# Optimization experiments

Hardware: AMD Instinct MI355X
Metric: run time of the kernel (lower is better)

## Reference

```python
import jax, jax.numpy as jnp
import numpy as np
from jax import lax

NX, NW, NY, NLAYER = 128, 64, 32, 2
NWUP, NBATCH, NHRZN = 256, 1024, 256


def setup_inputs() -> dict:
    key = jax.random.key(0)
    ks = jax.random.split(key, 18)
    s = 0.05
    n = lambda k, shp: jax.random.normal(k, shp, jnp.float32) * s
    return {
        "_Y0": jax.random.normal(ks[0], (NWUP + 1, NBATCH, NY), jnp.float32),
        # q_x_y: Linear(Ny, Nx*Nlayer) + Tanh
        "Wq": n(ks[1], (NX * NLAYER, NY)), "bq": n(ks[2], (NX * NLAYER,)),
        # p_y_x: Linear(Nx,Nx)+Tanh+Linear(Nx,Ny)
        "Wp1": n(ks[3], (NX, NX)), "bp1": n(ks[4], (NX,)),
        "Wp2": n(ks[5], (NY, NX)), "bp2": n(ks[6], (NY,)),
        # q_w_xy: Linear(Nx+Ny, Nw)+Tanh
        "Ww": n(ks[7], (NW, NX + NY)), "bw": n(ks[8], (NW,)),
        # GRU layer 0 (input Nw) and layer 1 (input Nx), PyTorch gate order r,z,n
        "Wih0": n(ks[9], (3 * NX, NW)), "Whh0": n(ks[10], (3 * NX, NX)),
        "bih0": n(ks[11], (3 * NX,)), "bhh0": n(ks[12], (3 * NX,)),
        "Wih1": n(ks[13], (3 * NX, NX)), "Whh1": n(ks[14], (3 * NX, NX)),
        "bih1": n(ks[15], (3 * NX,)), "bhh1": n(ks[16], (3 * NX,)),
        "Nhrzn": NHRZN,
    }


def _gru_cell(x, h, Wih, Whh, bih, bhh):
    # PyTorch GRUCell math, gate order (r, z, n)
    gi = x @ Wih.T + bih
    gh = h @ Whh.T + bhh
    ir, iz, inn = jnp.split(gi, 3, axis=-1)
    hr, hz, hn = jnp.split(gh, 3, axis=-1)
    r = jax.nn.sigmoid(ir + hr)
    z = jax.nn.sigmoid(iz + hz)
    ng = jnp.tanh(inn + r * hn)
    return (1.0 - z) * ng + z * h


def reference(_Y0, Wq, bq, Wp1, bp1, Wp2, bp2, Ww, bw,
              Wih0, Whh0, bih0, bhh0, Wih1, Whh1, bih1, bhh1, Nhrzn):
    Nwup = _Y0.shape[0] - 1
    B, Ny = _Y0.shape[1], _Y0.shape[2]
    Nlayer = Wq.shape[0] // Wp1.shape[0]
    Nx = Wp1.shape[0]

    p_y_x = lambda h: jnp.tanh(h @ Wp1.T + bp1) @ Wp2.T + bp2

    # initial multi-layer hidden state (Nlayer, B, Nx)
    x0 = jnp.tanh(_Y0[0] @ Wq.T + bq).reshape(B, Nlayer, Nx).transpose(1, 0, 2)
    yhat0 = p_y_x(x0[-1])

    T = Nwup + Nhrzn
    y_seq = jnp.concatenate(
        [_Y0[1:], jnp.zeros((Nhrzn, B, Ny), _Y0.dtype)], axis=0)  # (T, B, Ny)
    wup_mask = (jnp.arange(T) < Nwup).astype(_Y0.dtype)  # training branch: w=0 in horizon

    def step(carry, inp):
        x, yhat = carry  # x: (Nlayer, B, Nx)
        y_t, m = inp
        e = y_t - yhat
        w = jnp.tanh(jnp.concatenate([x[0], e], axis=-1) @ Ww.T + bw) * m
        h0 = _gru_cell(w, x[0], Wih0, Whh0, bih0, bhh0)
        h1 = _gru_cell(h0, x[1], Wih1, Whh1, bih1, bhh1)
        x_new = jnp.stack([h0, h1], axis=0)
        yhat_new = p_y_x(h1)
        return (x_new, yhat_new), (h1, w, yhat_new)

    _, (Xs, Ws, Ys) = lax.scan(step, (x0, yhat0), (y_seq, wup_mask))

    X = jnp.concatenate([x0[-1][None], Xs], axis=0)      # (T+1, B, Nx)
    Yhat = jnp.concatenate([yhat0[None], Ys], axis=0)    # (T+1, B, Ny)
    W = Ws[:Nwup]                                        # (Nwup, B, Nw)
    return X, W, Yhat
```

## Files before the change

kernel.cpp:

```cpp
#include <hip/hip_runtime.h>

#define NBATCH 1024
#define TSTEPS 512
#define NWUPC  256

#define XLEN 67239936ULL
#define WLEN 16777216ULL

typedef __attribute__((ext_vector_type(8))) short bf16x8;
typedef __attribute__((ext_vector_type(4))) float f32x4;

__device__ __forceinline__ unsigned short to_bf16u(float f) {
  union { float f; unsigned u; } v; v.f = f;
  unsigned r = (v.u + 0x7FFFu + ((v.u >> 16) & 1u)) >> 16;
  return (unsigned short)r;
}
__device__ __forceinline__ float bf16_to_f(short h) {
  union { unsigned u; float f; } v;
  v.u = ((unsigned)(unsigned short)h) << 16;
  return v.f;
}
__device__ __forceinline__ float sigm(float x) {
  x = fminf(fmaxf(x, -30.f), 30.f);
  return __builtin_amdgcn_rcpf(1.f + __expf(-x));
}
__device__ __forceinline__ float ftanh(float x) {
  x = fminf(fmaxf(x, -15.f), 15.f);
  float e = __expf(2.f * x);
  return (e - 1.f) * __builtin_amdgcn_rcpf(e + 1.f);
}

__device__ __forceinline__ void fast_barrier() {
  __builtin_amdgcn_sched_barrier(0);
  asm volatile("s_waitcnt lgkmcnt(0)" ::: "memory");
  __builtin_amdgcn_s_barrier();
  __builtin_amdgcn_sched_barrier(0);
}

#define MFMA16(a, b, c) __builtin_amdgcn_mfma_f32_16x16x32_bf16((a), (b), (c), 0, 0, 0)

__device__ __forceinline__ bf16x8 load_wfrag(const float* __restrict__ W, int ldk,
                                             int rowbase, int kbase, int cl, int rg) {
  const float* p = W + (size_t)(rowbase + cl) * (size_t)ldk + (size_t)(kbase + rg * 8);
  float4 a = *reinterpret_cast<const float4*>(p);
  float4 b = *reinterpret_cast<const float4*>(p + 4);
  bf16x8 r;
  r[0] = (short)to_bf16u(a.x); r[1] = (short)to_bf16u(a.y);
  r[2] = (short)to_bf16u(a.z); r[3] = (short)to_bf16u(a.w);
  r[4] = (short)to_bf16u(b.x); r[5] = (short)to_bf16u(b.y);
  r[6] = (short)to_bf16u(b.z); r[7] = (short)to_bf16u(b.w);
  return r;
}

template <int ROWB, int SLOTS>
__device__ __forceinline__ bf16x8 lds_afrag(const unsigned short* buf, int kt, int cl, int rg) {
  int chunk = (kt * 4 + rg) ^ (cl & (SLOTS - 1));
  return *reinterpret_cast<const bf16x8*>(
      reinterpret_cast<const char*>(buf) + cl * ROWB + chunk * 16);
}

template <int ROWB, int SLOTS>
__device__ __forceinline__ void store_c_lds(unsigned short* buf, int colbase, f32x4 v,
                                            int cl, int rg) {
#pragma unroll
  for (int r = 0; r < 4; ++r) {
    int row = rg * 4 + r;
    int col = colbase + cl;
    int chunk = (col >> 3) ^ (row & (SLOTS - 1));
    *reinterpret_cast<unsigned short*>(
        reinterpret_cast<char*>(buf) + row * ROWB + chunk * 16 + (col & 7) * 2) =
        to_bf16u(v[r]);
  }
}

__device__ __forceinline__ void store_c_glb(float* __restrict__ base, int ld, int colbase,
                                            f32x4 v, int cl, int rg) {
#pragma unroll
  for (int r = 0; r < 4; ++r) base[(rg * 4 + r) * ld + colbase + cl] = v[r];
}

__device__ __forceinline__ bf16x8 read_pfrag(const unsigned short* buf, int f, int lane) {
  return *reinterpret_cast<const bf16x8*>(buf + f * 512 + lane * 8);
}

__global__ __launch_bounds__(512, 2) void sinkbf_kernel(
    const float* __restrict__ Y0, const float* __restrict__ Wq, const float* __restrict__ bq,
    const float* __restrict__ Wp1, const float* __restrict__ bp1,
    const float* __restrict__ Wp2, const float* __restrict__ bp2,
    const float* __restrict__ Ww, const float* __restrict__ bw,
    const float* __restrict__ Wih0, const float* __restrict__ Whh0,
    const float* __restrict__ bih0, const float* __restrict__ bhh0,
    const float* __restrict__ Wih1, const float* __restrict__ Whh1,
    const float* __restrict__ bih1, const float* __restrict__ bhh1,
    float* __restrict__ outX, float* __restrict__ outW, float* __restrict__ outY) {
  const int tid = threadIdx.x;
  const int wid = tid >> 6;
  const int lane = tid & 63;
  const int cl = lane & 15;
  const int rg = lane >> 4;
  const int row0 = blockIdx.x * 16;
  const int c0 = wid * 16;

  __shared__ __align__(16) unsigned short sH0[2][16 * 128];
  __shared__ __align__(16) unsigned short sH1[2][16 * 128];
  __shared__ __align__(16) unsigned short sWb[16 * 64];
  __shared__ __align__(16) unsigned short sT[16 * 128];
  __shared__ __align__(16) unsigned short sYh[16 * 32];
  __shared__ __align__(16) unsigned short sWwP[20 * 512];
  __shared__ __align__(16) unsigned short sWp1P[32 * 512];
  __shared__ __align__(16) unsigned short sWp2P[8 * 512];

  const f32x4 vzero = {0.f, 0.f, 0.f, 0.f};

  bf16x8 wI0[3][2];
  bf16x8 wH0[3][4];
  bf16x8 wI1[3][4];
  bf16x8 wH1[3][4];
#pragma unroll
  for (int g = 0; g < 3; ++g) {
    int rb = g * 128 + c0;
#pragma unroll
    for (int kt = 0; kt < 2; ++kt) wI0[g][kt] = load_wfrag(Wih0, 64, rb, kt * 32, cl, rg);
#pragma unroll
    for (int kt = 0; kt < 4; ++kt) wH0[g][kt] = load_wfrag(Whh0, 128, rb, kt * 32, cl, rg);
#pragma unroll
    for (int kt = 0; kt < 4; ++kt) wI1[g][kt] = load_wfrag(Wih1, 128, rb, kt * 32, cl, rg);
#pragma unroll
    for (int kt = 0; kt < 4; ++kt) wH1[g][kt] = load_wfrag(Whh1, 128, rb, kt * 32, cl, rg);
  }

  if (wid < 4) {
#pragma unroll
    for (int kt = 0; kt < 5; ++kt) {
      bf16x8 f = load_wfrag(Ww, 160, wid * 16, kt * 32, cl, rg);
      *reinterpret_cast<bf16x8*>(&sWwP[(wid * 5 + kt) * 512 + lane * 8]) = f;
    }
  }
#pragma unroll
  for (int kt = 0; kt < 4; ++kt) {
    bf16x8 f = load_wfrag(Wp1, 128, c0, kt * 32, cl, rg);
    *reinterpret_cast<bf16x8*>(&sWp1P[(wid * 4 + kt) * 512 + lane * 8]) = f;
  }
  if (wid < 2) {
#pragma unroll
    for (int kt = 0; kt < 4; ++kt) {
      bf16x8 f = load_wfrag(Wp2, 128, wid * 16, kt * 32, cl, rg);
      *reinterpret_cast<bf16x8*>(&sWp2P[(wid * 4 + kt) * 512 + lane * 8]) = f;
    }
  }

  const int c = c0 + cl;
  const float b0r = bih0[c] + bhh0[c];
  const float b0z = bih0[128 + c] + bhh0[128 + c];
  const float b0in = bih0[256 + c];
  const float b0hn = bhh0[256 + c];
  const float b1r = bih1[c] + bhh1[c];
  const float b1z = bih1[128 + c] + bhh1[128 + c];
  const float b1in = bih1[256 + c];
  const float b1hn = bhh1[256 + c];
  const float bp1l = bp1[c];
  const float bwl = bw[(wid & 3) * 16 + cl];
  const float bp2l = (wid < 2) ? bp2[wid * 16 + cl] : 0.f;

  f32x4 hp0, hp1;

  {
    bf16x8 aY = load_wfrag(Y0, 32, row0, 0, cl, rg);
    bf16x8 q0 = load_wfrag(Wq, 32, c0, 0, cl, rg);
    bf16x8 q1 = load_wfrag(Wq, 32, 128 + c0, 0, cl, rg);
    float bq0v = bq[c];
    float bq1v = bq[128 + c];
    f32x4 acc = MFMA16(aY, q0, vzero);
#pragma unroll
    for (int r = 0; r < 4; ++r) hp0[r] = ftanh(acc[r] + bq0v);
    store_c_lds<256, 8>(sH0[0], c0, hp0, cl, rg);
    acc = MFMA16(aY, q1, vzero);
#pragma unroll
    for (int r = 0; r < 4; ++r) hp1[r] = ftanh(acc[r] + bq1v);
    store_c_lds<256, 8>(sH1[0], c0, hp1, cl, rg);
    store_c_glb(outX + (size_t)row0 * 128, 128, c0, hp1, cl, rg);
  }
  __syncthreads();

  float4 yA, yB;
  if (wid < 4) {
    const float* py = Y0 + (size_t)1 * (NBATCH * 32) + (size_t)(row0 + cl) * 32 + rg * 8;
    yA = *reinterpret_cast<const float4*>(py);
    yB = *reinterpret_cast<const float4*>(py + 4);
  }

  auto p_phase = [&](int tout, const unsigned short* h1buf) {
    bf16x8 a1[4];
#pragma unroll
    for (int kt = 0; kt < 4; ++kt) a1[kt] = lds_afrag<256, 8>(h1buf, kt, cl, rg);
    f32x4 acc = vzero;
#pragma unroll
    for (int kt = 0; kt < 4; ++kt)
      acc = MFMA16(a1[kt], read_pfrag(sWp1P, wid * 4 + kt, lane), acc);
    f32x4 tv;
#pragma unroll
    for (int r = 0; r < 4; ++r) tv[r] = ftanh(acc[r] + bp1l);
    store_c_lds<256, 8>(sT, c0, tv, cl, rg);
    fast_barrier();
    if (wid < 2) {
      bf16x8 at[4];
#pragma unroll
      for (int kt = 0; kt < 4; ++kt) at[kt] = lds_afrag<256, 8>(sT, kt, cl, rg);
      f32x4 acc2 = vzero;
#pragma unroll
      for (int kt = 0; kt < 4; ++kt) acc2 = MFMA16(at[kt], read_pfrag(sWp2P, wid * 4 + kt, lane), acc2);
      f32x4 y;
#pragma unroll
      for (int r = 0; r < 4; ++r) y[r] = acc2[r] + bp2l;
      store_c_glb(outY + (size_t)tout * (NBATCH * 32) + (size_t)row0 * 32, 32, wid * 16, y, cl, rg);
      store_c_lds<64, 4>(sYh, wid * 16, y, cl, rg);
    }
    fast_barrier();
  };

  p_phase(0, sH1[0]);

#pragma unroll 1
  for (int t = 0; t < TSTEPS; ++t) {
    const int cur = t & 1, nxt = cur ^ 1;
    const unsigned short* h0c = sH0[cur];
    unsigned short* h0w = sH0[nxt];
    const unsigned short* h1c = sH1[cur];
    unsigned short* h1w = sH1[nxt];
    const bool warm = (t < NWUPC);

    bf16x8 aH0[4];
#pragma unroll
    for (int kt = 0; kt < 4; ++kt) aH0[kt] = lds_afrag<256, 8>(h0c, kt, cl, rg);

    if (warm) {
      if (wid < 4) {
        bf16x8 ae;
        {
          int chunk = rg ^ (cl & 3);
          bf16x8 yh = *reinterpret_cast<const bf16x8*>(
              reinterpret_cast<const char*>(sYh) + cl * 64 + chunk * 16);
          ae[0] = (short)to_bf16u(yA.x - bf16_to_f(yh[0]));
          ae[1] = (short)to_bf16u(yA.y - bf16_to_f(yh[1]));
          ae[2] = (short)to_bf16u(yA.z - bf16_to_f(yh[2]));
          ae[3] = (short)to_bf16u(yA.w - bf16_to_f(yh[3]));
          ae[4] = (short)to_bf16u(yB.x - bf16_to_f(yh[4]));
          ae[5] = (short)to_bf16u(yB.y - bf16_to_f(yh[5]));
          ae[6] = (short)to_bf16u(yB.z - bf16_to_f(yh[6]));
          ae[7] = (short)to_bf16u(yB.w - bf16_to_f(yh[7]));
        }
        if (t + 1 < NWUPC) {
          const float* py = Y0 + (size_t)(2 + t) * (NBATCH * 32) + (size_t)(row0 + cl) * 32 + rg * 8;
          yA = *reinterpret_cast<const float4*>(py);
          yB = *reinterpret_cast<const float4*>(py + 4);
        }
        f32x4 acc = vzero;
#pragma unroll
        for (int kt = 0; kt < 4; ++kt)
          acc = MFMA16(aH0[kt], read_pfrag(sWwP, wid * 5 + kt, lane), acc);
        acc = MFMA16(ae, read_pfrag(sWwP, wid * 5 + 4, lane), acc);
        f32x4 wv;
#pragma unroll
        for (int r = 0; r < 4; ++r) wv[r] = ftanh(acc[r] + bwl);
        store_c_lds<128, 8>(sWb, wid * 16, wv, cl, rg);
        store_c_glb(outW + (size_t)t * (NBATCH * 64) + (size_t)row0 * 64, 64, wid * 16, wv, cl, rg);
      }
      fast_barrier();
    }

    f32x4 ar0 = vzero, az0 = vzero, ain0 = vzero, ahn0 = vzero;
    if (warm) {
      bf16x8 aw0 = lds_afrag<128, 8>(sWb, 0, cl, rg);
      bf16x8 aw1 = lds_afrag<128, 8>(sWb, 1, cl, rg);
      ar0 = MFMA16(aw0, wI0[0][0], ar0);  ar0 = MFMA16(aw1, wI0[0][1], ar0);
      az0 = MFMA16(aw0, wI0[1][0], az0);  az0 = MFMA16(aw1, wI0[1][1], az0);
      ain0 = MFMA16(aw0, wI0[2][0], ain0); ain0 = MFMA16(aw1, wI0[2][1], ain0);
    }
#pragma unroll
    for (int kt = 0; kt < 4; ++kt) {
      ar0 = MFMA16(aH0[kt], wH0[0][kt], ar0);
      az0 = MFMA16(aH0[kt], wH0[1][kt], az0);
      ahn0 = MFMA16(aH0[kt], wH0[2][kt], ahn0);
    }
    f32x4 h0new;
#pragma unroll
    for (int r = 0; r < 4; ++r) {
      float rr = sigm(ar0[r] + b0r);
      float zz = sigm(az0[r] + b0z);
      float ng = ftanh(ain0[r] + b0in + rr * (ahn0[r] + b0hn));
      h0new[r] = (1.f - zz) * ng + zz * hp0[r];
    }
    store_c_lds<256, 8>(h0w, c0, h0new, cl, rg);
    hp0 = h0new;
    fast_barrier();

    bf16x8 aH0n[4], aH1[4];
#pragma unroll
    for (int kt = 0; kt < 4; ++kt) aH0n[kt] = lds_afrag<256, 8>(h0w, kt, cl, rg);
#pragma unroll
    for (int kt = 0; kt < 4; ++kt) aH1[kt] = lds_afrag<256, 8>(h1c, kt, cl, rg);
    f32x4 ar1 = vzero, az1 = vzero, ain1 = vzero, ahn1 = vzero;
#pragma unroll
    for (int kt = 0; kt < 4; ++kt) {
      ar1 = MFMA16(aH0n[kt], wI1[0][kt], ar1);
      az1 = MFMA16(aH0n[kt], wI1[1][kt], az1);
      ain1 = MFMA16(aH0n[kt], wI1[2][kt], ain1);
      ar1 = MFMA16(aH1[kt], wH1[0][kt], ar1);
      az1 = MFMA16(aH1[kt], wH1[1][kt], az1);
      ahn1 = MFMA16(aH1[kt], wH1[2][kt], ahn1);
    }
    f32x4 h1new;
#pragma unroll
    for (int r = 0; r < 4; ++r) {
      float rr = sigm(ar1[r] + b1r);
      float zz = sigm(az1[r] + b1z);
      float ng = ftanh(ain1[r] + b1in + rr * (ahn1[r] + b1hn));
      h1new[r] = (1.f - zz) * ng + zz * hp1[r];
    }
    store_c_lds<256, 8>(h1w, c0, h1new, cl, rg);
    store_c_glb(outX + (size_t)(1 + t) * (NBATCH * 128) + (size_t)row0 * 128, 128,
                c0, h1new, cl, rg);
    hp1 = h1new;
    fast_barrier();

    if (warm) p_phase(1 + t, h1w);
  }
}

__global__ __launch_bounds__(256, 1) void yhat_hrzn_kernel(
    const float* __restrict__ X, const float* __restrict__ Wp1, const float* __restrict__ bp1,
    const float* __restrict__ Wp2, const float* __restrict__ bp2, float* __restrict__ outY) {
  const int tid = threadIdx.x;
  const int wid = tid >> 6;
  const int lane = tid & 63;
  const int cl = lane & 15;
  const int rg = lane >> 4;
  const int tile = blockIdx.x & 63;
  const int tg = blockIdx.x >> 6;
  const int row0 = tile * 16;
  const int c0 = wid * 32;

  __shared__ __align__(16) unsigned short sT2[2][16 * 128];
  const f32x4 vzero = {0.f, 0.f, 0.f, 0.f};

  bf16x8 wp1f[2][4];
#pragma unroll
  for (int tl = 0; tl < 2; ++tl)
#pragma unroll
    for (int kt = 0; kt < 4; ++kt) wp1f[tl][kt] = load_wfrag(Wp1, 128, c0 + tl * 16, kt * 32, cl, rg);
  bf16x8 wp2f[4];
  if (wid < 2) {
#pragma unroll
    for (int kt = 0; kt < 4; ++kt) wp2f[kt] = load_wfrag(Wp2, 128, wid * 16, kt * 32, cl, rg);
  } else {
#pragma unroll
    for (int kt = 0; kt < 4; ++kt) wp2f[kt] = bf16x8{0, 0, 0, 0, 0, 0, 0, 0};
  }
  float bp1l[2] = {bp1[c0 + cl], bp1[c0 + 16 + cl]};
  const float bp2l = (wid < 2) ? bp2[wid * 16 + cl] : 0.f;

#pragma unroll 1
  for (int i = 0; i < 4; ++i) {
    const int tt = 257 + tg * 4 + i;
    const float* xb = X + (size_t)tt * (NBATCH * 128);
    bf16x8 aX[4];
#pragma unroll
    for (int kt = 0; kt < 4; ++kt) aX[kt] = load_wfrag(xb, 128, row0, kt * 32, cl, rg);
#pragma unroll
    for (int tl = 0; tl < 2; ++tl) {
      f32x4 acc = vzero;
#pragma unroll
      for (int kt = 0; kt < 4; ++kt) acc = MFMA16(aX[kt], wp1f[tl][kt], acc);
      f32x4 tv;
#pragma unroll
      for (int r = 0; r < 4; ++r) tv[r] = ftanh(acc[r] + bp1l[tl]);
      store_c_lds<256, 8>(sT2[i & 1], c0 + tl * 16, tv, cl, rg);
    }
    __syncthreads();
    if (wid < 2) {
      bf16x8 at[4];
#pragma unroll
      for (int kt = 0; kt < 4; ++kt) at[kt] = lds_afrag<256, 8>(sT2[i & 1], kt, cl, rg);
      f32x4 acc = vzero;
#pragma unroll
      for (int kt = 0; kt < 4; ++kt) acc = MFMA16(at[kt], wp2f[kt], acc);
      f32x4 y;
#pragma unroll
      for (int r = 0; r < 4; ++r) y[r] = acc[r] + bp2l;
      store_c_glb(outY + (size_t)tt * (NBATCH * 32) + (size_t)row0 * 32, 32, wid * 16, y, cl, rg);
    }
  }
}

extern "C" void kernel_launch(void* const* d_in, const int* in_sizes, int n_in,
                              void* d_out, int out_size, void* d_ws, size_t ws_size,
                              hipStream_t stream) {
  (void)in_sizes; (void)n_in; (void)out_size; (void)d_ws; (void)ws_size;
  const float* Y0   = (const float*)d_in[0];
  const float* Wq   = (const float*)d_in[1];
  const float* bq   = (const float*)d_in[2];
  const float* Wp1  = (const float*)d_in[3];
  const float* bp1  = (const float*)d_in[4];
  const float* Wp2  = (const float*)d_in[5];
  const float* bp2  = (const float*)d_in[6];
  const float* Ww   = (const float*)d_in[7];
  const float* bw   = (const float*)d_in[8];
  const float* Wih0 = (const float*)d_in[9];
  const float* Whh0 = (const float*)d_in[10];
  const float* bih0 = (const float*)d_in[11];
  const float* bhh0 = (const float*)d_in[12];
  const float* Wih1 = (const float*)d_in[13];
  const float* Whh1 = (const float*)d_in[14];
  const float* bih1 = (const float*)d_in[15];
  const float* bhh1 = (const float*)d_in[16];

  float* outX = (float*)d_out;
  float* outW = outX + XLEN;
  float* outY = outW + WLEN;

  sinkbf_kernel<<<dim3(NBATCH / 16), dim3(512), 0, stream>>>(
      Y0, Wq, bq, Wp1, bp1, Wp2, bp2, Ww, bw,
      Wih0, Whh0, bih0, bhh0, Wih1, Whh1, bih1, bhh1,
      outX, outW, outY);

  yhat_hrzn_kernel<<<dim3(64 * 64), dim3(256), 0, stream>>>(
      outX, Wp1, bp1, Wp2, bp2, outY);
}
```

Before: 1.933 ms.

## Fold Wp2 into the innovation weight to cut yhat from the recurrent critical path

Because yhat is linear in the tanh hidden activation T, the error term e = y - yhat is rewritten algebraically. The Ww error block is premultiplied by -Wp2 and the bias is adjusted, so w is computed directly from y and T without first computing yhat. This removes the second Wp2 MFMA stage and one barrier from each recurrent step. The yhat output is now computed by spare waves 4-5 in parallel, and the horizon kernel picks up one extra timestep (with an extra block group and a bounds check). The trade-offs are a small change in bf16 rounding, a precompute of the folded weights at kernel start, and larger LDS use.

```diff
diff --git a/kernel.cpp b/kernel.cpp
--- a/kernel.cpp
+++ b/kernel.cpp
@@ -105,10 +105,8 @@
   __shared__ __align__(16) unsigned short sH1[2][16 * 128];
   __shared__ __align__(16) unsigned short sWb[16 * 64];
   __shared__ __align__(16) unsigned short sT[16 * 128];
-  __shared__ __align__(16) unsigned short sYh[16 * 32];
-  __shared__ __align__(16) unsigned short sWwP[20 * 512];
+  __shared__ __align__(16) unsigned short sWwP[36 * 512];
   __shared__ __align__(16) unsigned short sWp1P[32 * 512];
-  __shared__ __align__(16) unsigned short sWp2P[8 * 512];
 
   const f32x4 vzero = {0.f, 0.f, 0.f, 0.f};
 
@@ -131,9 +129,31 @@
 
   if (wid < 4) {
 #pragma unroll
-    for (int kt = 0; kt < 5; ++kt) {
+    for (int kt = 0; kt < 4; ++kt) {
       bf16x8 f = load_wfrag(Ww, 160, wid * 16, kt * 32, cl, rg);
-      *reinterpret_cast<bf16x8*>(&sWwP[(wid * 5 + kt) * 512 + lane * 8]) = f;
+      *reinterpret_cast<bf16x8*>(&sWwP[(wid * 9 + kt) * 512 + lane * 8]) = f;
+    }
+    {
+      bf16x8 f = load_wfrag(Ww, 160, wid * 16, 128, cl, rg);
+      *reinterpret_cast<bf16x8*>(&sWwP[(wid * 9 + 4) * 512 + lane * 8]) = f;
+    }
+    {
+      float wwc[32];
+#pragma unroll 8
+      for (int c = 0; c < 32; ++c) wwc[c] = Ww[(wid * 16 + cl) * 160 + 128 + c];
+#pragma unroll
+      for (int kt = 0; kt < 4; ++kt) {
+        bf16x8 f;
+#pragma unroll
+        for (int v = 0; v < 8; ++v) {
+          int k = kt * 32 + rg * 8 + v;
+          float s = 0.f;
+#pragma unroll 8
+          for (int c = 0; c < 32; ++c) s += Wp2[c * 128 + k] * wwc[c];
+          f[v] = (short)to_bf16u(-s);
+        }
+        *reinterpret_cast<bf16x8*>(&sWwP[(wid * 9 + 5 + kt) * 512 + lane * 8]) = f;
+      }
     }
   }
 #pragma unroll
@@ -141,12 +161,13 @@
     bf16x8 f = load_wfrag(Wp1, 128, c0, kt * 32, cl, rg);
     *reinterpret_cast<bf16x8*>(&sWp1P[(wid * 4 + kt) * 512 + lane * 8]) = f;
   }
-  if (wid < 2) {
-#pragma unroll
-    for (int kt = 0; kt < 4; ++kt) {
-      bf16x8 f = load_wfrag(Wp2, 128, wid * 16, kt * 32, cl, rg);
-      *reinterpret_cast<bf16x8*>(&sWp2P[(wid * 4 + kt) * 512 + lane * 8]) = f;
-    }
+  bf16x8 wp2f[4];
+  if (wid == 4 || wid == 5) {
+#pragma unroll
+    for (int kt = 0; kt < 4; ++kt) wp2f[kt] = load_wfrag(Wp2, 128, (wid - 4) * 16, kt * 32, cl, rg);
+  } else {
+#pragma unroll
+    for (int kt = 0; kt < 4; ++kt) wp2f[kt] = bf16x8{0, 0, 0, 0, 0, 0, 0, 0};
   }
 
   const int c = c0 + cl;
@@ -159,8 +180,14 @@
   const float b1in = bih1[256 + c];
   const float b1hn = bhh1[256 + c];
   const float bp1l = bp1[c];
-  const float bwl = bw[(wid & 3) * 16 + cl];
-  const float bp2l = (wid < 2) ? bp2[wid * 16 + cl] : 0.f;
+  float bwl = 0.f;
+  if (wid < 4) {
+    float s = bw[wid * 16 + cl];
+#pragma unroll 8
+    for (int cc = 0; cc < 32; ++cc) s -= bp2[cc] * Ww[(wid * 16 + cl) * 160 + 128 + cc];
+    bwl = s;
+  }
+  const float bp2l = (wid == 4 || wid == 5) ? bp2[(wid - 4) * 16 + cl] : 0.f;
 
   f32x4 hp0, hp1;
 
@@ -182,6 +209,20 @@
   }
   __syncthreads();
 
+  {
+    bf16x8 a1[4];
+#pragma unroll
+    for (int kt = 0; kt < 4; ++kt) a1[kt] = lds_afrag<256, 8>(sH1[0], kt, cl, rg);
+    f32x4 acc = vzero;
+#pragma unroll
+    for (int kt = 0; kt < 4; ++kt) acc = MFMA16(a1[kt], read_pfrag(sWp1P, wid * 4 + kt, lane), acc);
+    f32x4 tv;
+#pragma unroll
+    for (int r = 0; r < 4; ++r) tv[r] = ftanh(acc[r] + bp1l);
+    store_c_lds<256, 8>(sT, c0, tv, cl, rg);
+  }
+  fast_barrier();
+
   float4 yA, yB;
   if (wid < 4) {
     const float* py = Y0 + (size_t)1 * (NBATCH * 32) + (size_t)(row0 + cl) * 32 + rg * 8;
@@ -189,36 +230,9 @@
     yB = *reinterpret_cast<const float4*>(py + 4);
   }
 
-  auto p_phase = [&](int tout, const unsigned short* h1buf) {
-    bf16x8 a1[4];
-#pragma unroll
-    for (int kt = 0; kt < 4; ++kt) a1[kt] = lds_afrag<256, 8>(h1buf, kt, cl, rg);
-    f32x4 acc = vzero;
-#pragma unroll
-    for (int kt = 0; kt < 4; ++kt)
-      acc = MFMA16(a1[kt], read_pfrag(sWp1P, wid * 4 + kt, lane), acc);
-    f32x4 tv;
-#pragma unroll
-    for (int r = 0; r < 4; ++r) tv[r] = ftanh(acc[r] + bp1l);
-    store_c_lds<256, 8>(sT, c0, tv, cl, rg);
-    fast_barrier();
-    if (wid < 2) {
-      bf16x8 at[4];
-#pragma unroll
-      for (int kt = 0; kt < 4; ++kt) at[kt] = lds_afrag<256, 8>(sT, kt, cl, rg);
-      f32x4 acc2 = vzero;
-#pragma unroll
-      for (int kt = 0; kt < 4; ++kt) acc2 = MFMA16(at[kt], read_pfrag(sWp2P, wid * 4 + kt, lane), acc2);
-      f32x4 y;
-#pragma unroll
-      for (int r = 0; r < 4; ++r) y[r] = acc2[r] + bp2l;
-      store_c_glb(outY + (size_t)tout * (NBATCH * 32) + (size_t)row0 * 32, 32, wid * 16, y, cl, rg);
-      store_c_lds<64, 4>(sYh, wid * 16, y, cl, rg);
-    }
-    fast_barrier();
-  };
-
-  p_phase(0, sH1[0]);
+  float* pX = outX + (size_t)(NBATCH * 128) + (size_t)row0 * 128;
+  float* pW = outW + (size_t)row0 * 64;
+  float* pY = outY + (size_t)row0 * 32;
 
 #pragma unroll 1
   for (int t = 0; t < TSTEPS; ++t) {
@@ -235,58 +249,67 @@
 
     if (warm) {
       if (wid < 4) {
-        bf16x8 ae;
-        {
-          int chunk = rg ^ (cl & 3);
-          bf16x8 yh = *reinterpret_cast<const bf16x8*>(
-              reinterpret_cast<const char*>(sYh) + cl * 64 + chunk * 16);
-          ae[0] = (short)to_bf16u(yA.x - bf16_to_f(yh[0]));
-          ae[1] = (short)to_bf16u(yA.y - bf16_to_f(yh[1]));
-          ae[2] = (short)to_bf16u(yA.z - bf16_to_f(yh[2]));
-          ae[3] = (short)to_bf16u(yA.w - bf16_to_f(yh[3]));
-          ae[4] = (short)to_bf16u(yB.x - bf16_to_f(yh[4]));
-          ae[5] = (short)to_bf16u(yB.y - bf16_to_f(yh[5]));
-          ae[6] = (short)to_bf16u(yB.z - bf16_to_f(yh[6]));
-          ae[7] = (short)to_bf16u(yB.w - bf16_to_f(yh[7]));
-        }
+        bf16x8 tf[4];
+#pragma unroll
+        for (int kt = 0; kt < 4; ++kt) tf[kt] = lds_afrag<256, 8>(sT, kt, cl, rg);
+        bf16x8 ay;
+        ay[0] = (short)to_bf16u(yA.x); ay[1] = (short)to_bf16u(yA.y);
+        ay[2] = (short)to_bf16u(yA.z); ay[3] = (short)to_bf16u(yA.w);
+        ay[4] = (short)to_bf16u(yB.x); ay[5] = (short)to_bf16u(yB.y);
+        ay[6] = (short)to_bf16u(yB.z); ay[7] = (short)to_bf16u(yB.w);
         if (t + 1 < NWUPC) {
           const float* py = Y0 + (size_t)(2 + t) * (NBATCH * 32) + (size_t)(row0 + cl) * 32 + rg * 8;
           yA = *reinterpret_cast<const float4*>(py);
           yB = *reinterpret_cast<const float4*>(py + 4);
         }
+        f32x4 accA = MFMA16(ay, read_pfrag(sWwP, wid * 9 + 4, lane), vzero);
+#pragma unroll
+        for (int kt = 0; kt < 4; ++kt)
+          accA = MFMA16(aH0[kt], read_pfrag(sWwP, wid * 9 + kt, lane), accA);
+        f32x4 accB = vzero;
+#pragma unroll
+        for (int kt = 0; kt < 4; ++kt)
+          accB = MFMA16(tf[kt], read_pfrag(sWwP, wid * 9 + 5 + kt, lane), accB);
+        f32x4 wv;
+#pragma unroll
+        for (int r = 0; r < 4; ++r) wv[r] = ftanh(accA[r] + accB[r] + bwl);
+        store_c_lds<128, 8>(sWb, wid * 16, wv, cl, rg);
+        store_c_glb(pW, 64, wid * 16, wv, cl, rg);
+      } else if (wid < 6) {
+        bf16x8 tf[4];
+#pragma unroll
+        for (int kt = 0; kt < 4; ++kt) tf[kt] = lds_afrag<256, 8>(sT, kt, cl, rg);
         f32x4 acc = vzero;
 #pragma unroll
-        for (int kt = 0; kt < 4; ++kt)
-          acc = MFMA16(aH0[kt], read_pfrag(sWwP, wid * 5 + kt, lane), acc);
-        acc = MFMA16(ae, read_pfrag(sWwP, wid * 5 + 4, lane), acc);
-        f32x4 wv;
-#pragma unroll
-        for (int r = 0; r < 4; ++r) wv[r] = ftanh(acc[r] + bwl);
-        store_c_lds<128, 8>(sWb, wid * 16, wv, cl, rg);
-        store_c_glb(outW + (size_t)t * (NBATCH * 64) + (size_t)row0 * 64, 64, wid * 16, wv, cl, rg);
+        for (int kt = 0; kt < 4; ++kt) acc = MFMA16(tf[kt], wp2f[kt], acc);
+        f32x4 y;
+#pragma unroll
+        for (int r = 0; r < 4; ++r) y[r] = acc[r] + bp2l;
+        store_c_glb(pY, 32, (wid - 4) * 16, y, cl, rg);
       }
       fast_barrier();
     }
 
-    f32x4 ar0 = vzero, az0 = vzero, ain0 = vzero, ahn0 = vzero;
+    f32x4 ar0i = vzero, az0i = vzero, ain0 = vzero;
     if (warm) {
       bf16x8 aw0 = lds_afrag<128, 8>(sWb, 0, cl, rg);
       bf16x8 aw1 = lds_afrag<128, 8>(sWb, 1, cl, rg);
-      ar0 = MFMA16(aw0, wI0[0][0], ar0);  ar0 = MFMA16(aw1, wI0[0][1], ar0);
-      az0 = MFMA16(aw0, wI0[1][0], az0);  az0 = MFMA16(aw1, wI0[1][1], az0);
-      ain0 = MFMA16(aw0, wI0[2][0], ain0); ain0 = MFMA16(aw1, wI0[2][1], ain0);
-    }
+      ar0i = MFMA16(aw0, wI0[0][0], ar0i);  ar0i = MFMA16(aw1, wI0[0][1], ar0i);
+      az0i = MFMA16(aw0, wI0[1][0], az0i);  az0i = MFMA16(aw1, wI0[1][1], az0i);
+      ain0 = MFMA16(aw0, wI0[2][0], ain0);  ain0 = MFMA16(aw1, wI0[2][1], ain0);
+    }
+    f32x4 ar0h = vzero, az0h = vzero, ahn0 = vzero;
 #pragma unroll
     for (int kt = 0; kt < 4; ++kt) {
-      ar0 = MFMA16(aH0[kt], wH0[0][kt], ar0);
-      az0 = MFMA16(aH0[kt], wH0[1][kt], az0);
+      ar0h = MFMA16(aH0[kt], wH0[0][kt], ar0h);
+      az0h = MFMA16(aH0[kt], wH0[1][kt], az0h);
       ahn0 = MFMA16(aH0[kt], wH0[2][kt], ahn0);
     }
     f32x4 h0new;
 #pragma unroll
     for (int r = 0; r < 4; ++r) {
-      float rr = sigm(ar0[r] + b0r);
-      float zz = sigm(az0[r] + b0z);
+      float rr = sigm(ar0i[r] + ar0h[r] + b0r);
+      float zz = sigm(az0i[r] + az0h[r] + b0z);
       float ng = ftanh(ain0[r] + b0in + rr * (ahn0[r] + b0hn));
       h0new[r] = (1.f - zz) * ng + zz * hp0[r];
     }
@@ -299,31 +322,47 @@
     for (int kt = 0; kt < 4; ++kt) aH0n[kt] = lds_afrag<256, 8>(h0w, kt, cl, rg);
 #pragma unroll
     for (int kt = 0; kt < 4; ++kt) aH1[kt] = lds_afrag<256, 8>(h1c, kt, cl, rg);
-    f32x4 ar1 = vzero, az1 = vzero, ain1 = vzero, ahn1 = vzero;
+    f32x4 ar1i = vzero, az1i = vzero, ain1 = vzero;
+    f32x4 ar1h = vzero, az1h = vzero, ahn1 = vzero;
 #pragma unroll
     for (int kt = 0; kt < 4; ++kt) {
-      ar1 = MFMA16(aH0n[kt], wI1[0][kt], ar1);
-      az1 = MFMA16(aH0n[kt], wI1[1][kt], az1);
+      ar1i = MFMA16(aH0n[kt], wI1[0][kt], ar1i);
+      az1i = MFMA16(aH0n[kt], wI1[1][kt], az1i);
       ain1 = MFMA16(aH0n[kt], wI1[2][kt], ain1);
-      ar1 = MFMA16(aH1[kt], wH1[0][kt], ar1);
-      az1 = MFMA16(aH1[kt], wH1[1][kt], az1);
+      ar1h = MFMA16(aH1[kt], wH1[0][kt], ar1h);
+      az1h = MFMA16(aH1[kt], wH1[1][kt], az1h);
       ahn1 = MFMA16(aH1[kt], wH1[2][kt], ahn1);
     }
     f32x4 h1new;
 #pragma unroll
     for (int r = 0; r < 4; ++r) {
-      float rr = sigm(ar1[r] + b1r);
-      float zz = sigm(az1[r] + b1z);
+      float rr = sigm(ar1i[r] + ar1h[r] + b1r);
+      float zz = sigm(az1i[r] + az1h[r] + b1z);
       float ng = ftanh(ain1[r] + b1in + rr * (ahn1[r] + b1hn));
       h1new[r] = (1.f - zz) * ng + zz * hp1[r];
     }
     store_c_lds<256, 8>(h1w, c0, h1new, cl, rg);
-    store_c_glb(outX + (size_t)(1 + t) * (NBATCH * 128) + (size_t)row0 * 128, 128,
-                c0, h1new, cl, rg);
+    store_c_glb(pX, 128, c0, h1new, cl, rg);
     hp1 = h1new;
     fast_barrier();
 
-    if (warm) p_phase(1 + t, h1w);
+    if (t + 1 < NWUPC) {
+      bf16x8 a1[4];
+#pragma unroll
+      for (int kt = 0; kt < 4; ++kt) a1[kt] = lds_afrag<256, 8>(h1w, kt, cl, rg);
+      f32x4 acc = vzero;
+#pragma unroll
+      for (int kt = 0; kt < 4; ++kt) acc = MFMA16(a1[kt], read_pfrag(sWp1P, wid * 4 + kt, lane), acc);
+      f32x4 tv;
+#pragma unroll
+      for (int r = 0; r < 4; ++r) tv[r] = ftanh(acc[r] + bp1l);
+      store_c_lds<256, 8>(sT, c0, tv, cl, rg);
+      fast_barrier();
+    }
+
+    pX += NBATCH * 128;
+    pW += NBATCH * 64;
+    pY += NBATCH * 32;
   }
 }
 
@@ -361,7 +400,8 @@
 
 #pragma unroll 1
   for (int i = 0; i < 4; ++i) {
-    const int tt = 257 + tg * 4 + i;
+    const int tt = 256 + tg * 4 + i;
+    if (tt > 512) break;
     const float* xb = X + (size_t)tt * (NBATCH * 128);
     bf16x8 aX[4];
 #pragma unroll
@@ -389,6 +429,7 @@
       for (int r = 0; r < 4; ++r) y[r] = acc[r] + bp2l;
       store_c_glb(outY + (size_t)tt * (NBATCH * 32) + (size_t)row0 * 32, 32, wid * 16, y, cl, rg);
     }
+    __syncthreads();
   }
 }
 
@@ -423,6 +464,6 @@
       Wih0, Whh0, bih0, bhh0, Wih1, Whh1, bih1, bhh1,
       outX, outW, outY);
 
-  yhat_hrzn_kernel<<<dim3(64 * 64), dim3(256), 0, stream>>>(
+  yhat_hrzn_kernel<<<dim3(64 * 65), dim3(256), 0, stream>>>(
       outX, Wp1, bp1, Wp2, bp2, outY);
 }
```

Measured after the change: 2.031 ms. 5.1% more time.

## Split GRU gate accumulators and hoist h1 fragment loads off the critical path

Applied to the files above, without the earlier changes.

Moves the layer-1 hidden-state LDS fragment loads to the start of the step and splits the input and hidden gate accumulators into separate MFMA chains. This lets the h-dependent MFMAs issue before the barrier-gated input contributions are ready, shortening the serial dependency per step. It also drops the clamps in sigmoid/tanh, relaxes the sched_barrier masks around the block barrier, and replaces per-step output address arithmetic with incremented pointers. Removing the clamps risks inf/NaN handling edge cases, and the extra live fragment registers raise register pressure.

```diff
diff --git a/kernel.cpp b/kernel.cpp
--- a/kernel.cpp
+++ b/kernel.cpp
@@ -21,20 +21,17 @@
   return v.f;
 }
 __device__ __forceinline__ float sigm(float x) {
-  x = fminf(fmaxf(x, -30.f), 30.f);
   return __builtin_amdgcn_rcpf(1.f + __expf(-x));
 }
 __device__ __forceinline__ float ftanh(float x) {
-  x = fminf(fmaxf(x, -15.f), 15.f);
   float e = __expf(2.f * x);
   return (e - 1.f) * __builtin_amdgcn_rcpf(e + 1.f);
 }
 
 __device__ __forceinline__ void fast_barrier() {
-  __builtin_amdgcn_sched_barrier(0);
   asm volatile("s_waitcnt lgkmcnt(0)" ::: "memory");
   __builtin_amdgcn_s_barrier();
-  __builtin_amdgcn_sched_barrier(0);
+  __builtin_amdgcn_sched_barrier(0xF);
 }
 
 #define MFMA16(a, b, c) __builtin_amdgcn_mfma_f32_16x16x32_bf16((a), (b), (c), 0, 0, 0)
@@ -189,7 +186,11 @@
     yB = *reinterpret_cast<const float4*>(py + 4);
   }
 
-  auto p_phase = [&](int tout, const unsigned short* h1buf) {
+  float* pX = outX + (size_t)(NBATCH * 128) + (size_t)row0 * 128;
+  float* pW = outW + (size_t)row0 * 64;
+  float* pY = outY + (size_t)row0 * 32;
+
+  auto p_phase = [&](float* yout, const unsigned short* h1buf) {
     bf16x8 a1[4];
 #pragma unroll
     for (int kt = 0; kt < 4; ++kt) a1[kt] = lds_afrag<256, 8>(h1buf, kt, cl, rg);
@@ -212,13 +213,14 @@
       f32x4 y;
 #pragma unroll
       for (int r = 0; r < 4; ++r) y[r] = acc2[r] + bp2l;
-      store_c_glb(outY + (size_t)tout * (NBATCH * 32) + (size_t)row0 * 32, 32, wid * 16, y, cl, rg);
+      store_c_glb(yout, 32, wid * 16, y, cl, rg);
       store_c_lds<64, 4>(sYh, wid * 16, y, cl, rg);
     }
     fast_barrier();
   };
 
-  p_phase(0, sH1[0]);
+  p_phase(pY, sH1[0]);
+  pY += NBATCH * 32;
 
 #pragma unroll 1
   for (int t = 0; t < TSTEPS; ++t) {
@@ -229,9 +231,11 @@
     unsigned short* h1w = sH1[nxt];
     const bool warm = (t < NWUPC);
 
-    bf16x8 aH0[4];
+    bf16x8 aH0[4], aH1[4];
 #pragma unroll
     for (int kt = 0; kt < 4; ++kt) aH0[kt] = lds_afrag<256, 8>(h0c, kt, cl, rg);
+#pragma unroll
+    for (int kt = 0; kt < 4; ++kt) aH1[kt] = lds_afrag<256, 8>(h1c, kt, cl, rg);
 
     if (warm) {
       if (wid < 4) {
@@ -263,30 +267,31 @@
 #pragma unroll
         for (int r = 0; r < 4; ++r) wv[r] = ftanh(acc[r] + bwl);
         store_c_lds<128, 8>(sWb, wid * 16, wv, cl, rg);
-        store_c_glb(outW + (size_t)t * (NBATCH * 64) + (size_t)row0 * 64, 64, wid * 16, wv, cl, rg);
+        store_c_glb(pW, 64, wid * 16, wv, cl, rg);
       }
       fast_barrier();
     }
 
-    f32x4 ar0 = vzero, az0 = vzero, ain0 = vzero, ahn0 = vzero;
+    f32x4 ar0i = vzero, az0i = vzero, ain0 = vzero;
     if (warm) {
       bf16x8 aw0 = lds_afrag<128, 8>(sWb, 0, cl, rg);
       bf16x8 aw1 = lds_afrag<128, 8>(sWb, 1, cl, rg);
-      ar0 = MFMA16(aw0, wI0[0][0], ar0);  ar0 = MFMA16(aw1, wI0[0][1], ar0);
-      az0 = MFMA16(aw0, wI0[1][0], az0);  az0 = MFMA16(aw1, wI0[1][1], az0);
-      ain0 = MFMA16(aw0, wI0[2][0], ain0); ain0 = MFMA16(aw1, wI0[2][1], ain0);
-    }
+      ar0i = MFMA16(aw0, wI0[0][0], ar0i);  ar0i = MFMA16(aw1, wI0[0][1], ar0i);
+      az0i = MFMA16(aw0, wI0[1][0], az0i);  az0i = MFMA16(aw1, wI0[1][1], az0i);
+      ain0 = MFMA16(aw0, wI0[2][0], ain0);  ain0 = MFMA16(aw1, wI0[2][1], ain0);
+    }
+    f32x4 ar0h = vzero, az0h = vzero, ahn0 = vzero;
 #pragma unroll
     for (int kt = 0; kt < 4; ++kt) {
-      ar0 = MFMA16(aH0[kt], wH0[0][kt], ar0);
-      az0 = MFMA16(aH0[kt], wH0[1][kt], az0);
+      ar0h = MFMA16(aH0[kt], wH0[0][kt], ar0h);
+      az0h = MFMA16(aH0[kt], wH0[1][kt], az0h);
       ahn0 = MFMA16(aH0[kt], wH0[2][kt], ahn0);
     }
     f32x4 h0new;
 #pragma unroll
     for (int r = 0; r < 4; ++r) {
-      float rr = sigm(ar0[r] + b0r);
-      float zz = sigm(az0[r] + b0z);
+      float rr = sigm(ar0i[r] + ar0h[r] + b0r);
+      float zz = sigm(az0i[r] + az0h[r] + b0z);
       float ng = ftanh(ain0[r] + b0in + rr * (ahn0[r] + b0hn));
       h0new[r] = (1.f - zz) * ng + zz * hp0[r];
     }
@@ -294,36 +299,40 @@
     hp0 = h0new;
     fast_barrier();
 
-    bf16x8 aH0n[4], aH1[4];
+    bf16x8 aH0n[4];
 #pragma unroll
     for (int kt = 0; kt < 4; ++kt) aH0n[kt] = lds_afrag<256, 8>(h0w, kt, cl, rg);
-#pragma unroll
-    for (int kt = 0; kt < 4; ++kt) aH1[kt] = lds_afrag<256, 8>(h1c, kt, cl, rg);
-    f32x4 ar1 = vzero, az1 = vzero, ain1 = vzero, ahn1 = vzero;
+    f32x4 ar1i = vzero, az1i = vzero, ain1 = vzero;
+    f32x4 ar1h = vzero, az1h = vzero, ahn1 = vzero;
 #pragma unroll
     for (int kt = 0; kt < 4; ++kt) {
-      ar1 = MFMA16(aH0n[kt], wI1[0][kt], ar1);
-      az1 = MFMA16(aH0n[kt], wI1[1][kt], az1);
+      ar1h = MFMA16(aH1[kt], wH1[0][kt], ar1h);
+      az1h = MFMA16(aH1[kt], wH1[1][kt], az1h);
+      ahn1 = MFMA16(aH1[kt], wH1[2][kt], ahn1);
+      ar1i = MFMA16(aH0n[kt], wI1[0][kt], ar1i);
+      az1i = MFMA16(aH0n[kt], wI1[1][kt], az1i);
       ain1 = MFMA16(aH0n[kt], wI1[2][kt], ain1);
-      ar1 = MFMA16(aH1[kt], wH1[0][kt], ar1);
-      az1 = MFMA16(aH1[kt], wH1[1][kt], az1);
-      ahn1 = MFMA16(aH1[kt], wH1[2][kt], ahn1);
     }
     f32x4 h1new;
 #pragma unroll
     for (int r = 0; r < 4; ++r) {
-      float rr = sigm(ar1[r] + b1r);
-      float zz = sigm(az1[r] + b1z);
+      float rr = sigm(ar1i[r] + ar1h[r] + b1r);
+      float zz = sigm(az1i[r] + az1h[r] + b1z);
       float ng = ftanh(ain1[r] + b1in + rr * (ahn1[r] + b1hn));
       h1new[r] = (1.f - zz) * ng + zz * hp1[r];
     }
     store_c_lds<256, 8>(h1w, c0, h1new, cl, rg);
-    store_c_glb(outX + (size_t)(1 + t) * (NBATCH * 128) + (size_t)row0 * 128, 128,
-                c0, h1new, cl, rg);
+    store_c_glb(pX, 128, c0, h1new, cl, rg);
     hp1 = h1new;
     fast_barrier();
 
-    if (warm) p_phase(1 + t, h1w);
+    if (warm) {
+      p_phase(pY, h1w);
+    }
+
+    pX += NBATCH * 128;
+    pW += NBATCH * 64;
+    pY += NBATCH * 32;
   }
 }
 
```

Result: slower. 2.206 ms (+14.1%).
